# Kernel tuning notes

Hardware: AMD Instinct MI355X
Metric: run time of the kernel (lower is better)

Reference implementation:

```python
import jax, jax.numpy as jnp
import numpy as np

FP8_MAX = 448.0  # torch.finfo(torch.float8_e4m3fn).max
FP8_MIN = -448.0


def per_tensor_quantize(t):
    # amax = max(|min|, |max|) over the whole tensor
    amax = jnp.maximum(jnp.abs(jnp.min(t)), jnp.abs(jnp.max(t)))
    scale = FP8_MAX / jnp.clip(amax, 1e-12, None)
    q = jnp.clip(t * scale, FP8_MIN, FP8_MAX).astype(jnp.float8_e4m3fn)
    inv_scale = (1.0 / scale).astype(jnp.float32)
    return q, inv_scale


def setup_inputs() -> dict:
    key = jax.random.key(0)
    k1, k2 = jax.random.split(key)
    B, S, D_IN, D_OUT = 8, 8192, 1024, 1024
    x = jax.random.normal(k1, (B, S, D_IN), dtype=jnp.float32)
    w = jax.random.normal(k2, (D_OUT, D_IN), dtype=jnp.float32) * 0.02
    qweight, weight_scale = per_tensor_quantize(w)  # fp8 weight + scalar fp32 scale
    return {"x": x, "qweight": qweight, "weight_scale": weight_scale}


def reference(x, qweight, weight_scale):
    # dynamic per-tensor activation quantization (quantize -> fp8)
    qinput, act_scale = per_tensor_quantize(x)
    # fp8 gemm with inline dequant scales (manual dequant-linear path, bias=None)
    A = qinput.astype(x.dtype) * act_scale          # [B, S, D_in]
    W = qweight.astype(x.dtype) * weight_scale.astype(x.dtype)  # [D_out, D_in]
    out = jnp.einsum('bsk,nk->bsn', A, W)           # [B, S, D_out]
    return out
```

## Files before the change

kernel.cpp:

```cpp
#include <hip/hip_runtime.h>
#include <hip/hip_fp8.h>
#include <stdint.h>
#include <cmath>

using f32x4  = __attribute__((ext_vector_type(4)))  float;
using f32x16 = __attribute__((ext_vector_type(16))) float;
using i32x4  = __attribute__((ext_vector_type(4)))  int;
using i32x8  = __attribute__((ext_vector_type(8)))  int;

#define FP8MAX 448.0f

__device__ __forceinline__ void gload_lds16(const void* g, void* l) {
  __builtin_amdgcn_global_load_lds(
      (const __attribute__((address_space(1))) unsigned int*)g,
      (__attribute__((address_space(3))) unsigned int*)l,
      16, 0, 0);
}

__device__ __forceinline__ uint8_t to_fp8(float v) {
  __hip_fp8_e4m3 q(fminf(fmaxf(v, -FP8MAX), FP8MAX));
  return q.__x;
}

__device__ __forceinline__ uint32_t quant4(float4 v, float s) {
  return (uint32_t)to_fp8(v.x * s) | ((uint32_t)to_fp8(v.y * s) << 8) |
         ((uint32_t)to_fp8(v.z * s) << 16) | ((uint32_t)to_fp8(v.w * s) << 24);
}

__global__ void amax_wconv(const float* __restrict__ x, size_t n4,
                           unsigned int* __restrict__ amax_u,
                           const uint8_t* __restrict__ w,
                           uint8_t* __restrict__ qw, int n1) {
  if ((int)blockIdx.x * 1024 < n1) {
    const float* wf = (const float*)w;
    const unsigned short* wh = (const unsigned short*)w;
    int f32ok = 1, bf16ok = 1;
    for (int i = threadIdx.x; i < 4096; i += 256) {
      float v = wf[i];
      if (!(isfinite(v) && fabsf(v) <= FP8MAX)) f32ok = 0;
      else { __hip_fp8_e4m3 qq(v); if ((float)qq != v) f32ok = 0; }
      float hv = __uint_as_float(((unsigned int)wh[i]) << 16);
      if (!(isfinite(hv) && fabsf(hv) <= FP8MAX)) bf16ok = 0;
      else { __hip_fp8_e4m3 qh(hv); if ((float)qh != hv) bf16ok = 0; }
    }
    __shared__ int sf, sb;
    if (threadIdx.x == 0) { sf = 1; sb = 1; }
    __syncthreads();
    if (!f32ok) atomicAnd(&sf, 0);
    if (!bf16ok) atomicAnd(&sb, 0);
    __syncthreads();
    unsigned int f = sf ? 2u : (sb ? 1u : 0u);

    int i0 = (blockIdx.x * 256 + threadIdx.x) * 4;
    if (i0 < n1) {
      uint32_t out;
      if (f == 2) {
        float4 v = *(const float4*)((const float*)w + i0);
        out = (uint32_t)to_fp8(v.x) | ((uint32_t)to_fp8(v.y) << 8) |
              ((uint32_t)to_fp8(v.z) << 16) | ((uint32_t)to_fp8(v.w) << 24);
      } else if (f == 1) {
        ushort4 h = *(const ushort4*)((const unsigned short*)w + i0);
        out = (uint32_t)to_fp8(__uint_as_float(((unsigned int)h.x) << 16)) |
              ((uint32_t)to_fp8(__uint_as_float(((unsigned int)h.y) << 16)) << 8) |
              ((uint32_t)to_fp8(__uint_as_float(((unsigned int)h.z) << 16)) << 16) |
              ((uint32_t)to_fp8(__uint_as_float(((unsigned int)h.w) << 16)) << 24);
      } else {
        out = *(const uint32_t*)(w + i0);
      }
      *(uint32_t*)(qw + i0) = out;
    }
  }

  const float4* x4 = (const float4*)x;
  float m = 0.0f;
  size_t stride = (size_t)gridDim.x * blockDim.x;
  for (size_t i = (size_t)blockIdx.x * blockDim.x + threadIdx.x; i < n4; i += stride) {
    float4 v = x4[i];
    m = fmaxf(m, fmaxf(fmaxf(fabsf(v.x), fabsf(v.y)),
                       fmaxf(fabsf(v.z), fabsf(v.w))));
  }
  #pragma unroll
  for (int off = 32; off > 0; off >>= 1)
    m = fmaxf(m, __shfl_xor(m, off));
  __shared__ float sm[16];
  int wid = threadIdx.x >> 6;
  if ((threadIdx.x & 63) == 0) sm[wid] = m;
  __syncthreads();
  if (threadIdx.x == 0) {
    int nw = blockDim.x >> 6;
    float r = sm[0];
    for (int i = 1; i < nw; i++) r = fmaxf(r, sm[i]);
    atomicMax(amax_u, __float_as_uint(r));
  }
}

#define SROWS 64

__global__ __launch_bounds__(256, 2) void fused_gemm(
    const float* __restrict__ X,
    const uint8_t* __restrict__ B,
    float* __restrict__ C,
    const float* __restrict__ amax_p,
    const float* __restrict__ wscale_p) {
  __shared__ uint8_t qa[SROWS * 1024];
  __shared__ uint8_t qb[256 * 64];

  const int t = threadIdx.x;
  const int lane = t & 63;
  const int wave = t >> 6;

  const float amax = fmaxf(amax_p[0], 1e-12f);
  const float scale = FP8MAX / amax;
  const float s = (1.0f / scale) * wscale_p[0];

  const float4* x4 = (const float4*)(X + (size_t)blockIdx.x * (SROWS * 1024));
  #pragma unroll 4
  for (int i = 0; i < 64; ++i) {
    float4 v = x4[i * 256 + t];
    uint32_t wq = quant4(v, scale);
    int swc = (t >> 2) ^ (i & 15);
    *(uint32_t*)&qa[i * 1024 + swc * 16 + (t & 3) * 4] = wq;
  }

  const int lr = lane & 31;
  const int kh = lane >> 5;
  const int x15 = lr & 15;
  const int rsw = (lr >> 1) & 3;
  const int brow = t >> 2;
  const int gsw = ((t & 3) ^ ((t >> 3) & 3)) * 16;

  const size_t c_row0 = (size_t)blockIdx.x * SROWS;

  for (int n = 0; n < 4; ++n) {
    f32x16 acc[2][2] = {};
    for (int kt = 0; kt < 16; ++kt) {
      __syncthreads();
      #pragma unroll
      for (int p = 0; p < 4; ++p) {
        int r = brow + p * 64;
        gload_lds16(B + (size_t)(n * 256 + r) * 1024 + kt * 64 + gsw,
                    &qb[p * 4096 + t * 16]);
      }
      __syncthreads();

      i32x8 af[2], bf[2];
      #pragma unroll
      for (int i = 0; i < 2; i++) {
        const uint8_t* p = &qa[(i * 32 + lr) * 1024];
        int cb = kt * 4 + kh * 2;
        i32x4 lo = *(const i32x4*)(p + ((cb    ) ^ x15) * 16);
        i32x4 hi = *(const i32x4*)(p + ((cb + 1) ^ x15) * 16);
        af[i] = (i32x8){lo.x, lo.y, lo.z, lo.w, hi.x, hi.y, hi.z, hi.w};
      }
      #pragma unroll
      for (int j = 0; j < 2; j++) {
        const uint8_t* p = &qb[(wave * 64 + j * 32 + lr) * 64];
        i32x4 lo = *(const i32x4*)(p + ((2 * kh    ) ^ rsw) * 16);
        i32x4 hi = *(const i32x4*)(p + ((2 * kh + 1) ^ rsw) * 16);
        bf[j] = (i32x8){lo.x, lo.y, lo.z, lo.w, hi.x, hi.y, hi.z, hi.w};
      }
      __builtin_amdgcn_s_setprio(1);
      #pragma unroll
      for (int i = 0; i < 2; i++)
        #pragma unroll
        for (int j = 0; j < 2; j++)
          acc[i][j] = __builtin_amdgcn_mfma_scale_f32_32x32x64_f8f6f4(
              af[i], bf[j], acc[i][j],
              0 , 0 ,
              0, 0x7f7f7f7f,
              0, 0x7f7f7f7f);
      __builtin_amdgcn_s_setprio(0);
    }

    #pragma unroll
    for (int i = 0; i < 2; i++) {
      #pragma unroll
      for (int j = 0; j < 2; j++) {
        size_t row0 = c_row0 + i * 32 + (kh << 2);
        int col = n * 256 + wave * 64 + j * 32 + lr;
        #pragma unroll
        for (int r = 0; r < 16; r++) {
          size_t row = row0 + (r & 3) + ((r >> 2) << 3);
          C[row * 1024 + col] = acc[i][j][r] * s;
        }
      }
    }
  }
}

extern "C" void kernel_launch(void* const* d_in, const int* in_sizes, int n_in,
                              void* d_out, int out_size, void* d_ws, size_t ws_size,
                              hipStream_t stream) {
  const float* x = (const float*)d_in[0];
  const uint8_t* wraw = (const uint8_t*)d_in[1];
  const float* wscale = (const float*)d_in[2];
  float* out = (float*)d_out;

  long long in0 = in_sizes[0];
  long long in1 = in_sizes[1];
  double kd = sqrt((double)in0 * (double)in1 / (double)out_size);
  long long K = (long long)(kd + 0.5);
  long long M = in0 / K;

  unsigned int* amax_u = (unsigned int*)d_ws;
  const float* amax_f = (const float*)d_ws;
  uint8_t* qw = (uint8_t*)d_ws + 4096;

  hipMemsetAsync(d_ws, 0, 4, stream);
  amax_wconv<<<2048, 256, 0, stream>>>(x, (size_t)(in0 / 4), amax_u,
                                       wraw, qw, (int)in1);
  fused_gemm<<<(unsigned)(M / SROWS), 256, 0, stream>>>(x, qw, out,
                                                        amax_f, wscale);
}
```

Before: 233.3 us.

## Give each wave a private B tile and drop block-wide barriers in GEMM loop

Each wave now loads only the 64 B rows it consumes into its own LDS slice, so the two __syncthreads per k-step become per-wave s_waitcnt waits. The next step's B tile is issued right after the current fragments are read into registers, so the global-to-LDS copy overlaps the MFMAs. A single barrier after the A quantization remains. The risk is the explicit vmcnt/lgkmcnt ordering and single buffering: the next load may still stall behind the wait at the top of each iteration.

Result: slower. 892.9 us (+282.7%).

```diff
diff --git a/kernel.cpp b/kernel.cpp
--- a/kernel.cpp
+++ b/kernel.cpp
@@ -103,7 +103,7 @@
     const float* __restrict__ amax_p,
     const float* __restrict__ wscale_p) {
   __shared__ uint8_t qa[SROWS * 1024];
-  __shared__ uint8_t qb[256 * 64];
+  __shared__ uint8_t qb[4][4096];
 
   const int t = threadIdx.x;
   const int lane = t & 63;
@@ -121,29 +121,46 @@
     int swc = (t >> 2) ^ (i & 15);
     *(uint32_t*)&qa[i * 1024 + swc * 16 + (t & 3) * 4] = wq;
   }
+  __syncthreads();
 
   const int lr = lane & 31;
   const int kh = lane >> 5;
   const int x15 = lr & 15;
   const int rsw = (lr >> 1) & 3;
-  const int brow = t >> 2;
-  const int gsw = ((t & 3) ^ ((t >> 3) & 3)) * 16;
+  const int c0b = ((2 * kh) ^ rsw) << 4;
+  const int c1b = ((2 * kh + 1) ^ rsw) << 4;
+
+  uint8_t* qbw = qb[wave];
+  const int sgq = ((lane & 3) ^ ((lane >> 3) & 3)) * 16;
+  const int srl = lane >> 2;
+  const uint8_t* gb = B + (size_t)(wave * 64) * 1024 + sgq;
+
+  auto stage = [&](int step) {
+    int nn = step >> 4, kk = step & 15;
+    const uint8_t* g = gb + (size_t)(nn * 256) * 1024 + kk * 64;
+    #pragma unroll
+    for (int c = 0; c < 4; ++c)
+      gload_lds16(g + (size_t)(c * 16 + srl) * 1024, qbw + c * 1024 + lane * 16);
+  };
 
   const size_t c_row0 = (size_t)blockIdx.x * SROWS;
+
+  stage(0);
 
   for (int n = 0; n < 4; ++n) {
     f32x16 acc[2][2] = {};
     for (int kt = 0; kt < 16; ++kt) {
-      __syncthreads();
-      #pragma unroll
-      for (int p = 0; p < 4; ++p) {
-        int r = brow + p * 64;
-        gload_lds16(B + (size_t)(n * 256 + r) * 1024 + kt * 64 + gsw,
-                    &qb[p * 4096 + t * 16]);
-      }
-      __syncthreads();
+      const int step = n * 16 + kt;
+      asm volatile("s_waitcnt vmcnt(0)" ::: "memory");
 
       i32x8 af[2], bf[2];
+      #pragma unroll
+      for (int j = 0; j < 2; j++) {
+        const uint8_t* p = qbw + (j * 32 + lr) * 64;
+        i32x4 lo = *(const i32x4*)(p + c0b);
+        i32x4 hi = *(const i32x4*)(p + c1b);
+        bf[j] = (i32x8){lo.x, lo.y, lo.z, lo.w, hi.x, hi.y, hi.z, hi.w};
+      }
       #pragma unroll
       for (int i = 0; i < 2; i++) {
         const uint8_t* p = &qa[(i * 32 + lr) * 1024];
@@ -152,13 +169,10 @@
         i32x4 hi = *(const i32x4*)(p + ((cb + 1) ^ x15) * 16);
         af[i] = (i32x8){lo.x, lo.y, lo.z, lo.w, hi.x, hi.y, hi.z, hi.w};
       }
-      #pragma unroll
-      for (int j = 0; j < 2; j++) {
-        const uint8_t* p = &qb[(wave * 64 + j * 32 + lr) * 64];
-        i32x4 lo = *(const i32x4*)(p + ((2 * kh    ) ^ rsw) * 16);
-        i32x4 hi = *(const i32x4*)(p + ((2 * kh + 1) ^ rsw) * 16);
-        bf[j] = (i32x8){lo.x, lo.y, lo.z, lo.w, hi.x, hi.y, hi.z, hi.w};
-      }
+      asm volatile("s_waitcnt lgkmcnt(0)" ::: "memory");
+      __builtin_amdgcn_sched_barrier(0);
+      if (step + 1 < 64) stage(step + 1);
+
       __builtin_amdgcn_s_setprio(1);
       #pragma unroll
       for (int i = 0; i < 2; i++)
```
